# Optimization experiments

Measured on AMD Instinct MI355X. Metric: run time of the kernel, lower is better.

The kernel has to match this reference:

```python
import jax, jax.numpy as jnp
import numpy as np

FRAME_LENGTH = 800
FRAME_STEP = 200
FFT_LENGTH = 800


def _hann_window(n):
    # tf.signal.hann_window default: periodic=True -> 0.5 - 0.5*cos(2*pi*k/n)
    k = jnp.arange(n, dtype=jnp.float32)
    return 0.5 - 0.5 * jnp.cos(2.0 * np.pi * k / n)


def setup_inputs() -> dict:
    key = jax.random.key(0)
    signals = jax.random.normal(key, (16, 240000), dtype=jnp.float32)
    window = _hann_window(FRAME_LENGTH)  # fft_length == frame_length, no pad
    n = jnp.arange(FFT_LENGTH, dtype=jnp.float32)
    angles = -2.0 * np.pi * n[:, None] * n[None, :] / float(FFT_LENGTH)  # [k, n]
    dft_cos = jnp.cos(angles)
    dft_sin = jnp.sin(angles)
    return {"signals": signals, "window": window, "dft_cos": dft_cos, "dft_sin": dft_sin}


def reference(signals, window, dft_cos, dft_sin):
    # Frame the signal: [B, num_frames, frame_length] via gather (pad_end=False)
    signal_length = signals.shape[1]
    num_frames = (signal_length - FRAME_LENGTH) // FRAME_STEP + 1
    starts = jnp.arange(num_frames, dtype=jnp.int32) * FRAME_STEP
    offsets = jnp.arange(FRAME_LENGTH, dtype=jnp.int32)
    idx = starts[:, None] + offsets[None, :]          # [F, L]
    frames = signals[:, idx]                          # [B, F, L]
    windowed = frames * window[:FRAME_LENGTH]         # [B, F, L]
    # Dense real/imag DFT: out[b,f,k] = sum_n windowed[b,f,n] * dft[k,n]
    real = jnp.einsum('bfn,kn->bfk', windowed, dft_cos)
    imag = jnp.einsum('bfn,kn->bfk', windowed, dft_sin)
    bins = FFT_LENGTH // 2 + 1
    return jnp.stack([real[:, :, :bins], imag[:, :, :bins]], axis=-1)  # [B, F, bins, 2]
```

## Files before the change

kernel.cpp:

```cpp
#include <hip/hip_runtime.h>
#include <hip/hip_bf16.h>

#define NBATCH   16
#define SIGLEN   240000
#define FRAMES   1197
#define M_TOTAL  (NBATCH * FRAMES)
#define K_TOTAL  800
#define NBINS    401
#define NOUT     (2 * NBINS)
#define FSTEP    200

#define KPAD  832
#define NTK   26
#define GBN   64
#define GMB   1024
#define GNT   13
#define GMT   19
#define GNWG  (GNT * GMT)
#define BSTR  840

#define SIG_ELEMS  ((size_t)NBATCH * SIGLEN)
#define B_WS_ELEMS ((size_t)(GNT * GBN) * KPAD)
#define WS_NEEDED  ((SIG_ELEMS + B_WS_ELEMS) * 2)

#define PREP_SIG_BLOCKS 1875
#define PREP_B_BLOCKS   338

typedef float  f32x4  __attribute__((ext_vector_type(4)));
typedef __bf16 bf16x8 __attribute__((ext_vector_type(8)));

static __device__ __forceinline__ unsigned f2bf_pair(float lo, float hi) {
    union { float f; unsigned u; } a, b;
    a.f = lo; b.f = hi;
    unsigned ua = (a.u + 0x7fffu + ((a.u >> 16) & 1u)) >> 16;
    unsigned ub = (b.u + 0x7fffu + ((b.u >> 16) & 1u)) >> 16;
    return ua | (ub << 16);
}

__global__ __launch_bounds__(256) void prep_all(
    const float* __restrict__ sig, const float* __restrict__ wnd,
    const float* __restrict__ dcos, const float* __restrict__ dsin,
    ushort* __restrict__ sbf, ushort* __restrict__ B)
{
    const int blk = blockIdx.x;
    if (blk < PREP_SIG_BLOCKS) {
        size_t i8 = ((size_t)blk * 256 + threadIdx.x) * 8;
        const float4 s0 = *(const float4*)(sig + i8);
        const float4 s1 = *(const float4*)(sig + i8 + 4);
        uint4 p;
        p.x = f2bf_pair(s0.x, s0.y);
        p.y = f2bf_pair(s0.z, s0.w);
        p.z = f2bf_pair(s1.x, s1.y);
        p.w = f2bf_pair(s1.z, s1.w);
        *(uint4*)(sbf + i8) = p;
    } else {
        int idx = (blk - PREP_SIG_BLOCKS) * 256 + threadIdx.x;
        int j  = idx / 104;
        int c8 = (idx - j * 104) * 8;
        uint4 p;
        if (j < NOUT && c8 < K_TOTAL) {
            const float* src = ((j & 1) ? dsin : dcos) + (size_t)(j >> 1) * K_TOTAL + c8;
            const float4 s0 = *(const float4*)(src);
            const float4 s1 = *(const float4*)(src + 4);
            const float4 w0 = *(const float4*)(wnd + c8);
            const float4 w1 = *(const float4*)(wnd + c8 + 4);
            p.x = f2bf_pair(s0.x * w0.x, s0.y * w0.y);
            p.y = f2bf_pair(s0.z * w0.z, s0.w * w0.w);
            p.z = f2bf_pair(s1.x * w1.x, s1.y * w1.y);
            p.w = f2bf_pair(s1.z * w1.z, s1.w * w1.w);
        } else {
            p = make_uint4(0u, 0u, 0u, 0u);
        }
        *(uint4*)(B + (size_t)j * KPAD + c8) = p;
    }
}

__global__ __launch_bounds__(1024, 4) void stft_gemm_bp5(
    const ushort* __restrict__ sigbf, const ushort* __restrict__ Bw,
    float* __restrict__ out)
{
    __shared__ ushort Bs[GBN * BSTR];

    const int tid  = threadIdx.x;

    const int orig = blockIdx.x;
    const int xcd  = orig & 7;
    const int idx  = orig >> 3;
    const int lbid = (xcd < 7 ? xcd * 31 : 217 + (xcd - 7) * 30) + idx;

    const int ntile = lbid % GNT;
    const int mblk  = lbid / GNT;
    const int j0    = ntile * GBN;
    const int m0    = mblk * GMB;

    const int wave = tid >> 6;
    const int lane = tid & 63;
    const int lr   = lane & 15;
    const int lg   = lane >> 4;
    const int mrow = m0 + wave * 64;

    unsigned aOfs[4];
    #pragma unroll
    for (int i = 0; i < 4; ++i) {
        int row = mrow + i * 16 + lr;
        if (row >= M_TOTAL) row = M_TOTAL - 1;
        int bb = row / FRAMES, ff = row - bb * FRAMES;
        aOfs[i] = (unsigned)(bb * SIGLEN + ff * FSTEP + lg * 8);
    }
    const int bBase = lr * BSTR + lg * 8;

    f32x4 acc[4][4];
    #pragma unroll
    for (int i = 0; i < 4; ++i)
        #pragma unroll
        for (int jj = 0; jj < 4; ++jj)
            acc[i][jj] = (f32x4){0.f, 0.f, 0.f, 0.f};

#define LOADA(A_, step) do {                                        \
        const int kofs_ = (step) * 32;                              \
        _Pragma("unroll")                                           \
        for (int i = 0; i < 4; ++i)                                 \
            A_[i] = *(const bf16x8*)(sigbf + aOfs[i] + kofs_);      \
    } while (0)

#define LOADB(B_, step) do {                                        \
        const int kofs_ = (step) * 32;                              \
        _Pragma("unroll")                                           \
        for (int jj = 0; jj < 4; ++jj)                              \
            B_[jj] = *(const bf16x8*)&Bs[jj * (16 * BSTR) + bBase + kofs_]; \
    } while (0)

#define MM(A_, B_) do {                                             \
        __builtin_amdgcn_s_setprio(1);                              \
        _Pragma("unroll")                                           \
        for (int i = 0; i < 4; ++i)                                 \
            _Pragma("unroll")                                       \
            for (int jj = 0; jj < 4; ++jj)                          \
                acc[i][jj] = __builtin_amdgcn_mfma_f32_16x16x32_bf16( \
                    A_[i], B_[jj], acc[i][jj], 0, 0, 0);            \
        __builtin_amdgcn_s_setprio(0);                              \
    } while (0)

    bf16x8 aX[4], aY[4], bX[4];

    LOADA(aX, 0);
    LOADA(aY, 1);

    #pragma unroll
    for (int it = 0; it < 6; ++it) {
        int c   = tid + 1024 * it;
        int row = c / 104;
        int col = (c - row * 104) * 8;
        *(uint4*)&Bs[row * BSTR + col] =
            *(const uint4*)(Bw + (size_t)(j0 + row) * KPAD + col);
    }
    if (tid < 512) {
        int c   = tid + 6144;
        int row = c / 104;
        int col = (c - row * 104) * 8;
        *(uint4*)&Bs[row * BSTR + col] =
            *(const uint4*)(Bw + (size_t)(j0 + row) * KPAD + col);
    }
    __syncthreads();

    #pragma unroll 1
    for (int t = 0; t < NTK - 2; t += 2) {
        LOADB(bX, t);
        MM(aX, bX);
        LOADA(aX, t + 2);
        LOADB(bX, t + 1);
        MM(aY, bX);
        LOADA(aY, t + 3);
    }
    LOADB(bX, 24); MM(aX, bX);
    LOADB(bX, 25); MM(aY, bX);

#undef LOADA
#undef LOADB
#undef MM

    #pragma unroll
    for (int i = 0; i < 4; ++i) {
        #pragma unroll
        for (int jj = 0; jj < 4; ++jj) {
            int col = j0 + jj * 16 + lr;
            if (col >= NOUT) continue;
            #pragma unroll
            for (int r = 0; r < 4; ++r) {
                int row = mrow + i * 16 + lg * 4 + r;
                if (row < M_TOTAL)
                    out[(size_t)row * NOUT + col] = acc[i][jj][r];
            }
        }
    }
}

#define BM 128
#define BN 128
#define BK 32
#define NTILES_N 7
#define NTILES_M 150
#define NWG (NTILES_M * NTILES_N)
#define LDSS 40
__global__ __launch_bounds__(256) void stft_gemm_fb(
    const float* __restrict__ sig, const float* __restrict__ wnd,
    const float* __restrict__ dcos, const float* __restrict__ dsin,
    float* __restrict__ out)
{
    __shared__ ushort As[BM * LDSS];
    __shared__ ushort Bs[BN * LDSS];
    __shared__ int rowBase[BM];

    const int tid = threadIdx.x;
    const int bid = blockIdx.x;
    const int mt  = bid / NTILES_N;
    const int nt  = bid - mt * NTILES_N;
    const int m0  = mt * BM;
    const int j0  = nt * BN;

    if (tid < BM) {
        int m = m0 + tid;
        int v = -1;
        if (m < M_TOTAL) {
            int b  = m / FRAMES;
            int fl = m - b * FRAMES;
            v = b * SIGLEN + fl * FSTEP;
        }
        rowBase[tid] = v;
    }

    const int rS = tid >> 1;
    const int hS = tid & 1;

    const float* bRow = nullptr;
    {
        int j = j0 + rS;
        if (j < NOUT) {
            const float* srcm = (j & 1) ? dsin : dcos;
            bRow = srcm + (size_t)(j >> 1) * K_TOTAL;
        }
    }

    const int lane = tid & 63;
    const int wave = tid >> 6;
    const int wm   = wave >> 1;
    const int wn   = wave & 1;
    const int lr   = lane & 15;
    const int lg   = lane >> 4;

    f32x4 acc[4][4];
    #pragma unroll
    for (int i = 0; i < 4; ++i)
        #pragma unroll
        for (int jj = 0; jj < 4; ++jj)
            acc[i][jj] = (f32x4){0.f, 0.f, 0.f, 0.f};

    __syncthreads();

    for (int k0 = 0; k0 < K_TOTAL; k0 += BK) {
        {
            int base = rowBase[rS];
            float4 f0, f1, f2, f3;
            if (base >= 0) {
                const float4* sp = (const float4*)(sig + base + k0 + hS * 16);
                f0 = sp[0]; f1 = sp[1]; f2 = sp[2]; f3 = sp[3];
            } else {
                f0 = make_float4(0.f,0.f,0.f,0.f); f1 = f0; f2 = f0; f3 = f0;
            }
            const float4* wp = (const float4*)(wnd + k0 + hS * 16);
            float4 w0 = wp[0], w1 = wp[1], w2 = wp[2], w3 = wp[3];
            uint4 p0, p1;
            p0.x = f2bf_pair(f0.x * w0.x, f0.y * w0.y);
            p0.y = f2bf_pair(f0.z * w0.z, f0.w * w0.w);
            p0.z = f2bf_pair(f1.x * w1.x, f1.y * w1.y);
            p0.w = f2bf_pair(f1.z * w1.z, f1.w * w1.w);
            p1.x = f2bf_pair(f2.x * w2.x, f2.y * w2.y);
            p1.y = f2bf_pair(f2.z * w2.z, f2.w * w2.w);
            p1.z = f2bf_pair(f3.x * w3.x, f3.y * w3.y);
            p1.w = f2bf_pair(f3.z * w3.z, f3.w * w3.w);
            uint4* dst = (uint4*)&As[rS * LDSS + hS * 16];
            dst[0] = p0; dst[1] = p1;
        }
        {
            uint4 p0, p1;
            if (bRow) {
                const float4* sp = (const float4*)(bRow + k0 + hS * 16);
                float4 f0 = sp[0], f1 = sp[1], f2 = sp[2], f3 = sp[3];
                p0.x = f2bf_pair(f0.x, f0.y);
                p0.y = f2bf_pair(f0.z, f0.w);
                p0.z = f2bf_pair(f1.x, f1.y);
                p0.w = f2bf_pair(f1.z, f1.w);
                p1.x = f2bf_pair(f2.x, f2.y);
                p1.y = f2bf_pair(f2.z, f2.w);
                p1.z = f2bf_pair(f3.x, f3.y);
                p1.w = f2bf_pair(f3.z, f3.w);
            } else {
                p0 = make_uint4(0u,0u,0u,0u); p1 = p0;
            }
            uint4* dst = (uint4*)&Bs[rS * LDSS + hS * 16];
            dst[0] = p0; dst[1] = p1;
        }
        __syncthreads();

        bf16x8 a[4], b[4];
        #pragma unroll
        for (int i = 0; i < 4; ++i)
            a[i] = *(const bf16x8*)&As[(wm * 64 + i * 16 + lr) * LDSS + lg * 8];
        #pragma unroll
        for (int i = 0; i < 4; ++i)
            b[i] = *(const bf16x8*)&Bs[(wn * 64 + i * 16 + lr) * LDSS + lg * 8];
        #pragma unroll
        for (int i = 0; i < 4; ++i)
            #pragma unroll
            for (int jj = 0; jj < 4; ++jj)
                acc[i][jj] = __builtin_amdgcn_mfma_f32_16x16x32_bf16(a[i], b[jj], acc[i][jj], 0, 0, 0);

        __syncthreads();
    }

    const int mb = m0 + wm * 64;
    const int jb = j0 + wn * 64;
    #pragma unroll
    for (int i = 0; i < 4; ++i) {
        #pragma unroll
        for (int jj = 0; jj < 4; ++jj) {
            int col = jb + jj * 16 + lr;
            if (col >= NOUT) continue;
            #pragma unroll
            for (int r = 0; r < 4; ++r) {
                int row = mb + i * 16 + lg * 4 + r;
                if (row < M_TOTAL)
                    out[(size_t)row * NOUT + col] = acc[i][jj][r];
            }
        }
    }
}

extern "C" void kernel_launch(void* const* d_in, const int* in_sizes, int n_in,
                              void* d_out, int out_size, void* d_ws, size_t ws_size,
                              hipStream_t stream) {
    const float* sig  = (const float*)d_in[0];
    const float* wnd  = (const float*)d_in[1];
    const float* dcos = (const float*)d_in[2];
    const float* dsin = (const float*)d_in[3];
    float* out = (float*)d_out;

    if (ws_size >= WS_NEEDED && d_ws != nullptr) {
        ushort* sbf = (ushort*)d_ws;
        ushort* Bws = sbf + SIG_ELEMS;
        prep_all<<<dim3(PREP_SIG_BLOCKS + PREP_B_BLOCKS), dim3(256), 0, stream>>>(
            sig, wnd, dcos, dsin, sbf, Bws);
        stft_gemm_bp5<<<dim3(GNWG), dim3(1024), 0, stream>>>(sbf, Bws, out);
    } else {
        stft_gemm_fb<<<dim3(NWG), dim3(256), 0, stream>>>(sig, wnd, dcos, dsin, out);
    }
}
```

Measured before the change: 61.41 us.

## Pre-pack framed A tiles into MFMA fragment layout and use 512-thread GEMM

Adds a packing kernel that gathers the framed bf16 signal into a contiguous per-lane MFMA fragment layout, so the GEMM loads A with fully coalesced 16-byte reads instead of strided frame gathers. The new GEMM kernel uses 512 threads, with each wave covering 128 rows (8 row-fragments), and double-buffers A and B register fragments. The cost is an extra kernel launch and an extra write and read of about 32 MB of packed data, since overlapping frames are duplicated. It also needs a larger workspace; the old path remains as a fallback when the workspace is too small.

```diff
diff --git a/kernel.cpp b/kernel.cpp
--- a/kernel.cpp
+++ b/kernel.cpp
@@ -18,13 +18,18 @@
 #define GMT   19
 #define GNWG  (GNT * GMT)
 #define BSTR  840
+#define NRG   1197
 
 #define SIG_ELEMS  ((size_t)NBATCH * SIGLEN)
 #define B_WS_ELEMS ((size_t)(GNT * GBN) * KPAD)
-#define WS_NEEDED  ((SIG_ELEMS + B_WS_ELEMS) * 2)
+#define APK_ELEMS  ((size_t)NRG * NTK * 64 * 8)
+#define WS_TIER2   ((SIG_ELEMS + B_WS_ELEMS) * 2)
+#define WS_TIER1   ((SIG_ELEMS + B_WS_ELEMS + APK_ELEMS) * 2)
 
 #define PREP_SIG_BLOCKS 1875
 #define PREP_B_BLOCKS   338
+#define PACK_TOTAL (NRG * NTK * 64)
+#define PACK_BLOCKS ((PACK_TOTAL + 255) / 256)
 
 typedef float  f32x4  __attribute__((ext_vector_type(4)));
 typedef __bf16 bf16x8 __attribute__((ext_vector_type(8)));
@@ -75,6 +80,134 @@
     }
 }
 
+__global__ __launch_bounds__(256) void prep_pack(
+    const ushort* __restrict__ sbf, ushort* __restrict__ Apk)
+{
+    int idx = blockIdx.x * 256 + threadIdx.x;
+    if (idx >= PACK_TOTAL) return;
+    const int lane   = idx & 63;
+    const int kk     = (idx >> 6) % NTK;
+    const int rowgrp = idx / (64 * NTK);
+    const int row = rowgrp * 16 + (lane & 15);
+    const int bb  = row / FRAMES, ff = row - bb * FRAMES;
+    const ushort* src = sbf + (size_t)bb * SIGLEN + ff * FSTEP + kk * 32 + (lane >> 4) * 8;
+    *(uint4*)(Apk + (size_t)idx * 8) = *(const uint4*)src;
+}
+
+__global__ __launch_bounds__(512, 2) void stft_gemm_pk(
+    const ushort* __restrict__ Apk, const ushort* __restrict__ Bw,
+    float* __restrict__ out)
+{
+    __shared__ ushort Bs[GBN * BSTR];
+
+    const int tid  = threadIdx.x;
+
+    const int orig = blockIdx.x;
+    const int xcd  = orig & 7;
+    const int idx  = orig >> 3;
+    const int lbid = (xcd < 7 ? xcd * 31 : 217 + (xcd - 7) * 30) + idx;
+
+    const int ntile = lbid % GNT;
+    const int mblk  = lbid / GNT;
+    const int j0    = ntile * GBN;
+    const int m0    = mblk * GMB;
+
+    const int wave = tid >> 6;
+    const int lane = tid & 63;
+    const int lr   = lane & 15;
+    const int lg   = lane >> 4;
+    const int mrow = m0 + wave * 128;
+
+    const int g0 = (m0 >> 4) + wave * 8;
+    size_t aBase[8];
+    #pragma unroll
+    for (int i = 0; i < 8; ++i) {
+        int g = g0 + i;
+        if (g >= NRG) g = NRG - 1;
+        aBase[i] = (size_t)g * (NTK * 512) + lane * 8;
+    }
+
+    f32x4 acc[8][4];
+    #pragma unroll
+    for (int i = 0; i < 8; ++i)
+        #pragma unroll
+        for (int jj = 0; jj < 4; ++jj)
+            acc[i][jj] = (f32x4){0.f, 0.f, 0.f, 0.f};
+
+#define LOADA(A_, step) do {                                        \
+        _Pragma("unroll")                                           \
+        for (int i = 0; i < 8; ++i)                                 \
+            A_[i] = *(const bf16x8*)(Apk + aBase[i] + (step) * 512);\
+    } while (0)
+
+#define LOADB(B_, step) do {                                        \
+        const int kofs_ = (step) * 32;                              \
+        _Pragma("unroll")                                           \
+        for (int jj = 0; jj < 4; ++jj)                              \
+            B_[jj] = *(const bf16x8*)&Bs[jj * (16 * BSTR) + lr * BSTR + lg * 8 + kofs_]; \
+    } while (0)
+
+#define MM(A_, B_) do {                                             \
+        __builtin_amdgcn_s_setprio(1);                              \
+        _Pragma("unroll")                                           \
+        for (int i = 0; i < 8; ++i)                                 \
+            _Pragma("unroll")                                       \
+            for (int jj = 0; jj < 4; ++jj)                          \
+                acc[i][jj] = __builtin_amdgcn_mfma_f32_16x16x32_bf16( \
+                    A_[i], B_[jj], acc[i][jj], 0, 0, 0);            \
+        __builtin_amdgcn_s_setprio(0);                              \
+    } while (0)
+
+    bf16x8 aX[8], aY[8], bX[4], bY[4];
+
+    LOADA(aX, 0);
+    LOADA(aY, 1);
+
+    #pragma unroll
+    for (int it = 0; it < 13; ++it) {
+        int c   = tid + 512 * it;
+        int row = c / 104;
+        int col = (c - row * 104) * 8;
+        *(uint4*)&Bs[row * BSTR + col] =
+            *(const uint4*)(Bw + (size_t)(j0 + row) * KPAD + col);
+    }
+    __syncthreads();
+
+    LOADB(bX, 0);
+    LOADB(bY, 1);
+
+    #pragma unroll 1
+    for (int t = 0; t < NTK - 2; t += 2) {
+        MM(aX, bX);
+        LOADA(aX, t + 2);
+        LOADB(bX, t + 2);
+        MM(aY, bY);
+        LOADA(aY, t + 3);
+        LOADB(bY, t + 3);
+    }
+    MM(aX, bX);
+    MM(aY, bY);
+
+#undef LOADA
+#undef LOADB
+#undef MM
+
+    #pragma unroll
+    for (int i = 0; i < 8; ++i) {
+        #pragma unroll
+        for (int jj = 0; jj < 4; ++jj) {
+            int col = j0 + jj * 16 + lr;
+            if (col >= NOUT) continue;
+            #pragma unroll
+            for (int r = 0; r < 4; ++r) {
+                int row = mrow + i * 16 + lg * 4 + r;
+                if (row < M_TOTAL)
+                    out[(size_t)row * NOUT + col] = acc[i][jj][r];
+            }
+        }
+    }
+}
+
 __global__ __launch_bounds__(1024, 4) void stft_gemm_bp5(
     const ushort* __restrict__ sigbf, const ushort* __restrict__ Bw,
     float* __restrict__ out)
@@ -82,7 +215,6 @@
     __shared__ ushort Bs[GBN * BSTR];
 
     const int tid  = threadIdx.x;
-
     const int orig = blockIdx.x;
     const int xcd  = orig & 7;
     const int idx  = orig >> 3;
@@ -345,7 +477,15 @@
     const float* dsin = (const float*)d_in[3];
     float* out = (float*)d_out;
 
-    if (ws_size >= WS_NEEDED && d_ws != nullptr) {
+    if (ws_size >= WS_TIER1 && d_ws != nullptr) {
+        ushort* sbf = (ushort*)d_ws;
+        ushort* Bws = sbf + SIG_ELEMS;
+        ushort* Apk = Bws + B_WS_ELEMS;
+        prep_all<<<dim3(PREP_SIG_BLOCKS + PREP_B_BLOCKS), dim3(256), 0, stream>>>(
+            sig, wnd, dcos, dsin, sbf, Bws);
+        prep_pack<<<dim3(PACK_BLOCKS), dim3(256), 0, stream>>>(sbf, Apk);
+        stft_gemm_pk<<<dim3(GNWG), dim3(512), 0, stream>>>(Apk, Bws, out);
+    } else if (ws_size >= WS_TIER2 && d_ws != nullptr) {
         ushort* sbf = (ushort*)d_ws;
         ushort* Bws = sbf + SIG_ELEMS;
         prep_all<<<dim3(PREP_SIG_BLOCKS + PREP_B_BLOCKS), dim3(256), 0, stream>>>(
```

New measurement: 63.72 us. 1.04x slower.
